# Optimization experiments

Measured on AMD Instinct MI355X. Metric: run time of the kernel, lower is better.

## Reference

```python
import jax, jax.numpy as jnp
import numpy as np

B, T, C, H, L = 1024, 20, 512, 8, 8
V, BS = 2, 32
D = C // H
EPS = 1e-5


def setup_inputs() -> dict:
    key = jax.random.key(0)
    ks = iter(jax.random.split(key, 16))
    n = lambda shape, s=0.02: jax.random.normal(next(ks), shape, dtype=jnp.float32) * s
    return {
        "x": jax.random.normal(next(ks), (B, T, V), dtype=jnp.float32),
        "enc_w": n((V, C)), "enc_b": jnp.zeros((C,), jnp.float32),
        "wpe": n((BS, C)),
        "ln1_w": jnp.ones((L, C), jnp.float32), "ln1_b": jnp.zeros((L, C), jnp.float32),
        "attn_w": n((L, C, 3 * C)), "attn_b": jnp.zeros((L, 3 * C), jnp.float32),
        "proj_w": n((L, C, C), 0.02 / np.sqrt(2 * L)), "proj_b": jnp.zeros((L, C), jnp.float32),
        "ln2_w": jnp.ones((L, C), jnp.float32), "ln2_b": jnp.zeros((L, C), jnp.float32),
        "fc1_w": n((L, C, 4 * C)), "fc1_b": jnp.zeros((L, 4 * C), jnp.float32),
        "fc2_w": n((L, 4 * C, C), 0.02 / np.sqrt(2 * L)), "fc2_b": jnp.zeros((L, C), jnp.float32),
        "lnf_w": jnp.ones((C,), jnp.float32), "lnf_b": jnp.zeros((C,), jnp.float32),
        "pred_w": n((C, V)), "pred_b": jnp.zeros((V,), jnp.float32),
    }


def _ln(x, w, b):
    mu = x.mean(-1, keepdims=True)
    var = x.var(-1, keepdims=True)  # biased, matches torch LayerNorm
    return (x - mu) * jax.lax.rsqrt(var + EPS) * w + b


def _forward(x, enc_w, enc_b, wpe, ln1_w, ln1_b, attn_w, attn_b, proj_w, proj_b,
             ln2_w, ln2_b, fc1_w, fc1_b, fc2_w, fc2_b, lnf_w, lnf_b, pred_w, pred_b):
    # traj_encoder_1 + positional embeddings (pos = arange(1, T+1), T != 9)
    h = x @ enc_w + enc_b + wpe[1:T + 1]
    mask = jnp.tril(jnp.ones((T, T), bool))  # causal mask
    scale = 1.0 / np.sqrt(D)

    def block(h, p):
        l1w, l1b, aw, ab, pw, pb, l2w, l2b, f1w, f1b, f2w, f2b = p
        qkv = _ln(h, l1w, l1b) @ aw + ab          # [B,T,3C]
        q, k, v = jnp.split(qkv, 3, axis=-1)
        q = q.reshape(B, T, H, D).transpose(0, 2, 1, 3)
        k = k.reshape(B, T, H, D).transpose(0, 2, 1, 3)
        v = v.reshape(B, T, H, D).transpose(0, 2, 1, 3)
        att = jnp.einsum('bhqd,bhkd->bhqk', q, k) * scale
        att = jnp.where(mask, att, -jnp.inf)
        att = jax.nn.softmax(att, axis=-1)
        y = jnp.einsum('bhqk,bhkd->bhqd', att, v)
        y = y.transpose(0, 2, 1, 3).reshape(B, T, C)
        h = h + y @ pw + pb
        m = _ln(h, l2w, l2b)
        h = h + jax.nn.gelu(m @ f1w + f1b, approximate=False) @ f2w + f2b
        return h, None

    params = (ln1_w, ln1_b, attn_w, attn_b, proj_w, proj_b,
              ln2_w, ln2_b, fc1_w, fc1_b, fc2_w, fc2_b)
    h, _ = jax.lax.scan(block, h, params)
    feat = _ln(h, lnf_w, lnf_b)
    return feat @ pred_w + pred_b  # predictor_1 -> [B,T,2]


def reference(x, enc_w, enc_b, wpe, ln1_w, ln1_b, attn_w, attn_b, proj_w, proj_b,
              ln2_w, ln2_b, fc1_w, fc1_b, fc2_w, fc2_b, lnf_w, lnf_b, pred_w, pred_b):
    return _forward(x, enc_w, enc_b, wpe, ln1_w, ln1_b, attn_w, attn_b, proj_w, proj_b,
                    ln2_w, ln2_b, fc1_w, fc1_b, fc2_w, fc2_b, lnf_w, lnf_b, pred_w, pred_b)
```

## Files before the change

### kernel.cpp

```cpp
#include <hip/hip_runtime.h>
#include <hip/hip_bf16.h>
#include <math.h>

#define NB 1024
#define NT 20
#define NC 512
#define NH 8
#define NL 8
#define MTOK (NB*NT)

using bf16 = __hip_bfloat16;
typedef float f32x4 __attribute__((ext_vector_type(4)));
typedef short s16x8 __attribute__((ext_vector_type(8)));

static __device__ __forceinline__ float us2f(unsigned short u) {
    union { float f; unsigned int i; } c; c.i = ((unsigned int)u) << 16; return c.f;
}
static __device__ __forceinline__ unsigned short f2bfu(float x) {
    union { bf16 b; unsigned short u; } c; c.b = __float2bfloat16(x); return c.u;
}
static __device__ __forceinline__ bf16 f2bf(float x) { return __float2bfloat16(x); }

static __device__ __forceinline__ void cp16(const bf16* g, bf16* lds_base, int lane) {
#if __has_builtin(__builtin_amdgcn_global_load_lds)
    __builtin_amdgcn_global_load_lds(
        (const __attribute__((address_space(1))) unsigned int*)g,
        (__attribute__((address_space(3))) unsigned int*)lds_base, 16, 0, 0);
#else
    ((int4*)lds_base)[lane] = *(const int4*)g;
#endif
}

static __device__ __forceinline__ void sync_sched() {
#if __has_builtin(__builtin_amdgcn_sched_barrier)
    __builtin_amdgcn_sched_barrier(0);
#endif
}

static __device__ __forceinline__ float gelu_f(float v) {
    return v * __builtin_amdgcn_rcpf(
        1.0f + __expf(-1.5957691f * v * (1.0f + 0.044715f * v * v)));
}

__global__ __launch_bounds__(256) void enc_kernel(
    const float* __restrict__ x, const float* __restrict__ ew,
    const float* __restrict__ eb, const float* __restrict__ wpe,
    float* __restrict__ h) {
    int idx = blockIdx.x * 256 + threadIdx.x;
    int token = idx >> 7, c4 = idx & 127;
    int t = token % NT;
    float x0 = x[(size_t)token * 2], x1 = x[(size_t)token * 2 + 1];
    const float4* w4 = (const float4*)ew;
    float4 w0 = w4[c4], w1 = w4[128 + c4];
    float4 b = ((const float4*)eb)[c4];
    float4 pe = ((const float4*)(wpe + (size_t)(t + 1) * NC))[c4];
    float4 o;
    o.x = x0 * w0.x + x1 * w1.x + b.x + pe.x;
    o.y = x0 * w0.y + x1 * w1.y + b.y + pe.y;
    o.z = x0 * w0.z + x1 * w1.z + b.z + pe.z;
    o.w = x0 * w0.w + x1 * w1.w + b.w + pe.w;
    ((float4*)h)[idx] = o;
}

__global__ __launch_bounds__(256) void wconv_kernel(
    const float* __restrict__ in, bf16* __restrict__ out, int K, int N) {
    __shared__ float tile[32][33];
    int z = blockIdx.z;
    int k0 = blockIdx.x * 32, n0 = blockIdx.y * 32;
    int tx = threadIdx.x & 31, ty = threadIdx.x >> 5;
    const float* src = in + (size_t)z * K * N;
    bf16* dst = out + (size_t)z * K * N;
#pragma unroll
    for (int i = 0; i < 4; ++i)
        tile[ty + i * 8][tx] = src[(size_t)(k0 + ty + i * 8) * N + n0 + tx];
    __syncthreads();
#pragma unroll
    for (int i = 0; i < 4; ++i)
        dst[(size_t)(n0 + ty + i * 8) * K + k0 + tx] = f2bf(tile[tx][ty + i * 8]);
}

__global__ __launch_bounds__(256) void ln_kernel(
    const float* __restrict__ h, const float* __restrict__ w,
    const float* __restrict__ b, bf16* __restrict__ out) {
    int lane = threadIdx.x & 63, wave = threadIdx.x >> 6;
    int token = blockIdx.x * 4 + wave;
    const float4* row = (const float4*)(h + (size_t)token * NC);
    float4 v0 = row[lane], v1 = row[lane + 64];
    float s  = v0.x + v0.y + v0.z + v0.w + v1.x + v1.y + v1.z + v1.w;
    float sq = v0.x*v0.x + v0.y*v0.y + v0.z*v0.z + v0.w*v0.w
             + v1.x*v1.x + v1.y*v1.y + v1.z*v1.z + v1.w*v1.w;
#pragma unroll
    for (int off = 32; off; off >>= 1) {
        s  += __shfl_xor(s, off, 64);
        sq += __shfl_xor(sq, off, 64);
    }
    float mean = s * (1.0f / NC);
    float var = sq * (1.0f / NC) - mean * mean;
    float rstd = rsqrtf(var + 1e-5f);
    const float4* w4 = (const float4*)w;
    const float4* b4 = (const float4*)b;
    float4 wa = w4[lane], wb = w4[lane + 64];
    float4 ba = b4[lane], bb = b4[lane + 64];
    ushort4 o0, o1;
    o0.x = f2bfu((v0.x - mean) * rstd * wa.x + ba.x);
    o0.y = f2bfu((v0.y - mean) * rstd * wa.y + ba.y);
    o0.z = f2bfu((v0.z - mean) * rstd * wa.z + ba.z);
    o0.w = f2bfu((v0.w - mean) * rstd * wa.w + ba.w);
    o1.x = f2bfu((v1.x - mean) * rstd * wb.x + bb.x);
    o1.y = f2bfu((v1.y - mean) * rstd * wb.y + bb.y);
    o1.z = f2bfu((v1.z - mean) * rstd * wb.z + bb.z);
    o1.w = f2bfu((v1.w - mean) * rstd * wb.w + bb.w);
    *(ushort4*)(out + (size_t)token * NC + lane * 4) = o0;
    *(ushort4*)(out + (size_t)token * NC + 256 + lane * 4) = o1;
}

__global__ __launch_bounds__(256) void addln_kernel(
    float* __restrict__ h, const bf16* __restrict__ delta,
    const float* __restrict__ w, const float* __restrict__ b,
    bf16* __restrict__ out) {
    int lane = threadIdx.x & 63, wave = threadIdx.x >> 6;
    int token = blockIdx.x * 4 + wave;
    float4* row = (float4*)(h + (size_t)token * NC);
    float4 v0 = row[lane], v1 = row[lane + 64];
    const ushort4* drow = (const ushort4*)(delta + (size_t)token * NC);
    ushort4 d0 = drow[lane], d1 = drow[lane + 64];
    v0.x += us2f(d0.x); v0.y += us2f(d0.y); v0.z += us2f(d0.z); v0.w += us2f(d0.w);
    v1.x += us2f(d1.x); v1.y += us2f(d1.y); v1.z += us2f(d1.z); v1.w += us2f(d1.w);
    row[lane] = v0; row[lane + 64] = v1;
    float s  = v0.x + v0.y + v0.z + v0.w + v1.x + v1.y + v1.z + v1.w;
    float sq = v0.x*v0.x + v0.y*v0.y + v0.z*v0.z + v0.w*v0.w
             + v1.x*v1.x + v1.y*v1.y + v1.z*v1.z + v1.w*v1.w;
#pragma unroll
    for (int off = 32; off; off >>= 1) {
        s  += __shfl_xor(s, off, 64);
        sq += __shfl_xor(sq, off, 64);
    }
    float mean = s * (1.0f / NC);
    float var = sq * (1.0f / NC) - mean * mean;
    float rstd = rsqrtf(var + 1e-5f);
    const float4* w4 = (const float4*)w;
    const float4* b4 = (const float4*)b;
    float4 wa = w4[lane], wb = w4[lane + 64];
    float4 ba = b4[lane], bb = b4[lane + 64];
    ushort4 o0, o1;
    o0.x = f2bfu((v0.x - mean) * rstd * wa.x + ba.x);
    o0.y = f2bfu((v0.y - mean) * rstd * wa.y + ba.y);
    o0.z = f2bfu((v0.z - mean) * rstd * wa.z + ba.z);
    o0.w = f2bfu((v0.w - mean) * rstd * wa.w + ba.w);
    o1.x = f2bfu((v1.x - mean) * rstd * wb.x + bb.x);
    o1.y = f2bfu((v1.y - mean) * rstd * wb.y + bb.y);
    o1.z = f2bfu((v1.z - mean) * rstd * wb.z + bb.z);
    o1.w = f2bfu((v1.w - mean) * rstd * wb.w + bb.w);
    *(ushort4*)(out + (size_t)token * NC + lane * 4) = o0;
    *(ushort4*)(out + (size_t)token * NC + 256 + lane * 4) = o1;
}

template <int EPI>
__global__ __launch_bounds__(256) void gemm_a(
    const bf16* __restrict__ A, const bf16* __restrict__ Wt,
    const float* __restrict__ bias, bf16* __restrict__ outb, int N, int K) {
    __shared__ __align__(16) bf16 lB[2][128 * 32];
    const int tid = threadIdx.x;
    const int lane = tid & 63;
    const int wave = tid >> 6;

    const int flat = blockIdx.y * gridDim.x + blockIdx.x;
    const int per = (gridDim.x * gridDim.y) >> 3;
    const int nid = (flat & 7) * per + (flat >> 3);
    const int mt = nid / gridDim.x;
    const int nt = nid - mt * gridDim.x;
    const int m0 = mt * 128, n0 = nt * 128;

    f32x4 acc[2][8] = {};

    const int c0 = tid, c1 = tid + 256;
    const int r0 = c0 >> 2, q0 = (((c0 & 3) ^ ((r0 >> 1) & 3)) * 8);
    const int r1 = c1 >> 2, q1 = (((c1 & 3) ^ ((r1 >> 1) & 3)) * 8);
    const bf16* Bb = Wt + (size_t)n0 * K;

    const int fm = lane & 15;
    const int fk8 = (lane >> 4) * 8;
    const int fkS = (((lane >> 4) ^ ((fm >> 1) & 3)) * 8);
    const int iters = K / 32;

    const bf16* Arow0 = A + (size_t)(m0 + wave * 32 + fm) * K + fk8;
    const bf16* Arow1 = Arow0 + (size_t)16 * K;

    auto stageB = [&](int kk, int buf) {
        cp16(Bb + (size_t)r0 * K + kk + q0, &lB[buf][(wave * 64) * 8], lane);
        cp16(Bb + (size_t)r1 * K + kk + q1, &lB[buf][(256 + wave * 64) * 8], lane);
    };
    s16x8 a0 = *(const s16x8*)Arow0;
    s16x8 a1 = *(const s16x8*)Arow1;
    stageB(0, 0);
    for (int it = 0; it < iters; ++it) {
        const int cur = it & 1;
        const int kn = (it + 1 < iters) ? (it + 1) * 32 : 0;
        __builtin_amdgcn_s_barrier();
        s16x8 an0 = *(const s16x8*)(Arow0 + kn);
        s16x8 an1 = *(const s16x8*)(Arow1 + kn);
        stageB(kn, cur ^ 1);
        sync_sched();
        __builtin_amdgcn_s_waitcnt(0xF74);
        __builtin_amdgcn_s_barrier();
        sync_sched();

        s16x8 bfr[8];
#pragma unroll
        for (int ni = 0; ni < 8; ++ni)
            bfr[ni] = *(const s16x8*)&lB[cur][(ni * 16 + fm) * 32 + fkS];
#pragma unroll
        for (int ni = 0; ni < 8; ++ni)
            acc[0][ni] = __builtin_amdgcn_mfma_f32_16x16x32_bf16(a0, bfr[ni], acc[0][ni], 0, 0, 0);
#pragma unroll
        for (int ni = 0; ni < 8; ++ni)
            acc[1][ni] = __builtin_amdgcn_mfma_f32_16x16x32_bf16(a1, bfr[ni], acc[1][ni], 0, 0, 0);
        a0 = an0; a1 = an1;
    }

    const int er = lane >> 4;
    const int ec = lane & 15;
#pragma unroll
    for (int mi = 0; mi < 2; ++mi) {
#pragma unroll
        for (int ni = 0; ni < 8; ++ni) {
            int col = n0 + ni * 16 + ec;
            float bcol = bias[col];
#pragma unroll
            for (int r = 0; r < 4; ++r) {
                int row = m0 + wave * 32 + mi * 16 + er * 4 + r;
                float v = acc[mi][ni][r] + bcol;
                size_t idx = (size_t)row * N + col;
                if (EPI == 0) outb[idx] = f2bf(v);
                else          outb[idx] = f2bf(gelu_f(v));
            }
        }
    }
}

__global__ __launch_bounds__(256) void gemm64_a(
    const bf16* __restrict__ A, const bf16* __restrict__ Wt,
    const float* __restrict__ bias, bf16* __restrict__ outb, int N, int K) {
    __shared__ __align__(16) bf16 lB[2][64 * 32];
    const int tid = threadIdx.x;
    const int lane = tid & 63;
    const int wave = tid >> 6;

    const int flat = blockIdx.y * gridDim.x + blockIdx.x;
    const int per = (gridDim.x * gridDim.y) >> 3;
    const int nid = (flat & 7) * per + (flat >> 3);
    const int mt = nid / gridDim.x;
    const int nt = nid - mt * gridDim.x;
    const int m0 = mt * 128, n0 = nt * 64;

    f32x4 acc[2][4] = {};

    const int c0 = tid;
    const int r0 = c0 >> 2, q0 = (((c0 & 3) ^ ((r0 >> 1) & 3)) * 8);
    const bf16* Bb = Wt + (size_t)n0 * K;

    const int fm = lane & 15;
    const int fk8 = (lane >> 4) * 8;
    const int fkS = (((lane >> 4) ^ ((fm >> 1) & 3)) * 8);
    const int iters = K / 32;

    const bf16* Arow0 = A + (size_t)(m0 + wave * 32 + fm) * K + fk8;
    const bf16* Arow1 = Arow0 + (size_t)16 * K;

    auto stageB = [&](int kk, int buf) {
        cp16(Bb + (size_t)r0 * K + kk + q0, &lB[buf][(wave * 64) * 8], lane);
    };
    s16x8 a0 = *(const s16x8*)Arow0;
    s16x8 a1 = *(const s16x8*)Arow1;
    stageB(0, 0);
    for (int it = 0; it < iters; ++it) {
        const int cur = it & 1;
        const int kn = (it + 1 < iters) ? (it + 1) * 32 : 0;
        __builtin_amdgcn_s_barrier();
        s16x8 an0 = *(const s16x8*)(Arow0 + kn);
        s16x8 an1 = *(const s16x8*)(Arow1 + kn);
        stageB(kn, cur ^ 1);
        sync_sched();
        __builtin_amdgcn_s_waitcnt(0xF73);
        __builtin_amdgcn_s_barrier();
        sync_sched();

        s16x8 bfr[4];
#pragma unroll
        for (int ni = 0; ni < 4; ++ni)
            bfr[ni] = *(const s16x8*)&lB[cur][(ni * 16 + fm) * 32 + fkS];
#pragma unroll
        for (int ni = 0; ni < 4; ++ni)
            acc[0][ni] = __builtin_amdgcn_mfma_f32_16x16x32_bf16(a0, bfr[ni], acc[0][ni], 0, 0, 0);
#pragma unroll
        for (int ni = 0; ni < 4; ++ni)
            acc[1][ni] = __builtin_amdgcn_mfma_f32_16x16x32_bf16(a1, bfr[ni], acc[1][ni], 0, 0, 0);
        a0 = an0; a1 = an1;
    }

    const int er = lane >> 4;
    const int ec = lane & 15;
#pragma unroll
    for (int mi = 0; mi < 2; ++mi) {
#pragma unroll
        for (int ni = 0; ni < 4; ++ni) {
            int col = n0 + ni * 16 + ec;
            float bcol = bias[col];
#pragma unroll
            for (int r = 0; r < 4; ++r) {
                int row = m0 + wave * 32 + mi * 16 + er * 4 + r;
                float v = acc[mi][ni][r] + bcol;
                outb[(size_t)row * N + col] = f2bf(v);
            }
        }
    }
}

__global__ __launch_bounds__(64) void attn_kernel(
    const bf16* __restrict__ qkv, bf16* __restrict__ y) {
    __shared__ __align__(16) float qs[NT][68];
    __shared__ __align__(16) float ks[NT][68];
    __shared__ float vT[64][21];
    __shared__ __align__(16) float P[NT][24];
    const int lane = threadIdx.x;
    const int b = blockIdx.x >> 3, hh = blockIdx.x & 7;
    const bf16* base = qkv + (size_t)b * NT * (3 * NC) + hh * 64;

    for (int idx = lane; idx < NT * 32; idx += 64) {
        int t = idx >> 5, d2 = (idx & 31) * 2;
        const unsigned short* p;
        p = (const unsigned short*)(base + (size_t)t * (3 * NC) + d2);
        qs[t][d2] = us2f(p[0]); qs[t][d2 + 1] = us2f(p[1]);
        p = (const unsigned short*)(base + (size_t)t * (3 * NC) + NC + d2);
        ks[t][d2] = us2f(p[0]); ks[t][d2 + 1] = us2f(p[1]);
        p = (const unsigned short*)(base + (size_t)t * (3 * NC) + 2 * NC + d2);
        vT[d2][t] = us2f(p[0]); vT[d2 + 1][t] = us2f(p[1]);
    }
    __syncthreads();

    for (int pp = lane; pp < NT * NT; pp += 64) {
        int i = (int)(((unsigned)pp * 52429u) >> 20);
        int j = pp - i * 20;
        const float4* qi = (const float4*)qs[i];
        const float4* kj = (const float4*)ks[j];
        float s = 0.0f;
#pragma unroll
        for (int d4 = 0; d4 < 16; ++d4) {
            float4 a = qi[d4], c = kj[d4];
            s += a.x * c.x + a.y * c.y + a.z * c.z + a.w * c.w;
        }
        P[i][j] = s * 0.125f;
    }
    __syncthreads();

    if (lane < NT) {
        int i = lane;
        float m = -INFINITY;
        for (int j = 0; j <= i; ++j) m = fmaxf(m, P[i][j]);
        float sum = 0.0f;
        for (int j = 0; j <= i; ++j) { float e = __expf(P[i][j] - m); P[i][j] = e; sum += e; }
        float inv = 1.0f / sum;
        for (int j = 0; j <= i; ++j) P[i][j] *= inv;
        for (int j = i + 1; j < NT; ++j) P[i][j] = 0.0f;
    }
    __syncthreads();

    float vr[NT];
#pragma unroll
    for (int j = 0; j < NT; ++j) vr[j] = vT[lane][j];
    bf16* yb = y + (size_t)b * NT * NC + hh * 64;
#pragma unroll
    for (int i = 0; i < NT; ++i) {
        const float4* pr = (const float4*)P[i];
        float o = 0.0f;
#pragma unroll
        for (int j4 = 0; j4 < 5; ++j4) {
            float4 pv = pr[j4];
            o += pv.x * vr[j4 * 4] + pv.y * vr[j4 * 4 + 1]
               + pv.z * vr[j4 * 4 + 2] + pv.w * vr[j4 * 4 + 3];
        }
        yb[(size_t)i * NC + lane] = f2bf(o);
    }
}

__global__ __launch_bounds__(256) void lnf_pred_kernel(
    const float* __restrict__ h, const bf16* __restrict__ delta,
    const float* __restrict__ w, const float* __restrict__ b,
    const float* __restrict__ pw, const float* __restrict__ pb,
    float* __restrict__ out) {
    int lane = threadIdx.x & 63, wave = threadIdx.x >> 6;
    int token = blockIdx.x * 4 + wave;
    const float4* row = (const float4*)(h + (size_t)token * NC);
    float4 v0 = row[lane], v1 = row[lane + 64];
    const ushort4* drow = (const ushort4*)(delta + (size_t)token * NC);
    ushort4 d0 = drow[lane], d1 = drow[lane + 64];
    v0.x += us2f(d0.x); v0.y += us2f(d0.y); v0.z += us2f(d0.z); v0.w += us2f(d0.w);
    v1.x += us2f(d1.x); v1.y += us2f(d1.y); v1.z += us2f(d1.z); v1.w += us2f(d1.w);
    float s  = v0.x + v0.y + v0.z + v0.w + v1.x + v1.y + v1.z + v1.w;
    float sq = v0.x*v0.x + v0.y*v0.y + v0.z*v0.z + v0.w*v0.w
             + v1.x*v1.x + v1.y*v1.y + v1.z*v1.z + v1.w*v1.w;
#pragma unroll
    for (int off = 32; off; off >>= 1) {
        s  += __shfl_xor(s, off, 64);
        sq += __shfl_xor(sq, off, 64);
    }
    float mean = s * (1.0f / NC);
    float var = sq * (1.0f / NC) - mean * mean;
    float rstd = rsqrtf(var + 1e-5f);
    const float4* w4 = (const float4*)w;
    const float4* b4 = (const float4*)b;
    float4 wa = w4[lane], wb = w4[lane + 64];
    float4 ba = b4[lane], bb = b4[lane + 64];
    const float2* pw2 = (const float2*)pw;
    float a0 = 0.0f, a1 = 0.0f;
    int c = lane * 4;
    float f; float2 pv;
    f = (v0.x - mean) * rstd * wa.x + ba.x; pv = pw2[c + 0]; a0 += f * pv.x; a1 += f * pv.y;
    f = (v0.y - mean) * rstd * wa.y + ba.y; pv = pw2[c + 1]; a0 += f * pv.x; a1 += f * pv.y;
    f = (v0.z - mean) * rstd * wa.z + ba.z; pv = pw2[c + 2]; a0 += f * pv.x; a1 += f * pv.y;
    f = (v0.w - mean) * rstd * wa.w + ba.w; pv = pw2[c + 3]; a0 += f * pv.x; a1 += f * pv.y;
    c = 256 + lane * 4;
    f = (v1.x - mean) * rstd * wb.x + bb.x; pv = pw2[c + 0]; a0 += f * pv.x; a1 += f * pv.y;
    f = (v1.y - mean) * rstd * wb.y + bb.y; pv = pw2[c + 1]; a0 += f * pv.x; a1 += f * pv.y;
    f = (v1.z - mean) * rstd * wb.z + bb.z; pv = pw2[c + 2]; a0 += f * pv.x; a1 += f * pv.y;
    f = (v1.w - mean) * rstd * wb.w + bb.w; pv = pw2[c + 3]; a0 += f * pv.x; a1 += f * pv.y;
#pragma unroll
    for (int off = 32; off; off >>= 1) {
        a0 += __shfl_xor(a0, off, 64);
        a1 += __shfl_xor(a1, off, 64);
    }
    if (lane == 0) {
        out[(size_t)token * 2]     = a0 + pb[0];
        out[(size_t)token * 2 + 1] = a1 + pb[1];
    }
}

extern "C" void kernel_launch(void* const* d_in, const int* in_sizes, int n_in,
                              void* d_out, int out_size, void* d_ws, size_t ws_size,
                              hipStream_t stream) {
    (void)in_sizes; (void)n_in; (void)out_size; (void)ws_size;
    const float* x      = (const float*)d_in[0];
    const float* enc_w  = (const float*)d_in[1];
    const float* enc_b  = (const float*)d_in[2];
    const float* wpe    = (const float*)d_in[3];
    const float* ln1_w  = (const float*)d_in[4];
    const float* ln1_b  = (const float*)d_in[5];
    const float* attn_w = (const float*)d_in[6];
    const float* attn_b = (const float*)d_in[7];
    const float* proj_w = (const float*)d_in[8];
    const float* proj_b = (const float*)d_in[9];
    const float* ln2_w  = (const float*)d_in[10];
    const float* ln2_b  = (const float*)d_in[11];
    const float* fc1_w  = (const float*)d_in[12];
    const float* fc1_b  = (const float*)d_in[13];
    const float* fc2_w  = (const float*)d_in[14];
    const float* fc2_b  = (const float*)d_in[15];
    const float* lnf_w  = (const float*)d_in[16];
    const float* lnf_b  = (const float*)d_in[17];
    const float* pred_w = (const float*)d_in[18];
    const float* pred_b = (const float*)d_in[19];
    float* out = (float*)d_out;

    char* p = (char*)d_ws;
    float* h  = (float*)p;  p += (size_t)MTOK * NC * 4;
    bf16* xa  = (bf16*)p;   p += (size_t)MTOK * NC * 2;
    bf16* dl  = (bf16*)p;   p += (size_t)MTOK * NC * 2;
    bf16* big = (bf16*)p;   p += (size_t)MTOK * (4 * NC) * 2;
    bf16* aT  = (bf16*)p;   p += (size_t)NL * (3 * NC) * NC * 2;
    bf16* pT  = (bf16*)p;   p += (size_t)NL * NC * NC * 2;
    bf16* f1T = (bf16*)p;   p += (size_t)NL * (4 * NC) * NC * 2;
    bf16* f2T = (bf16*)p;   p += (size_t)NL * NC * (4 * NC) * 2;

    enc_kernel<<<MTOK * 128 / 256, 256, 0, stream>>>(x, enc_w, enc_b, wpe, h);
    wconv_kernel<<<dim3(16, 48, NL), 256, 0, stream>>>(attn_w, aT, NC, 3 * NC);
    wconv_kernel<<<dim3(16, 16, NL), 256, 0, stream>>>(proj_w, pT, NC, NC);
    wconv_kernel<<<dim3(16, 64, NL), 256, 0, stream>>>(fc1_w, f1T, NC, 4 * NC);
    wconv_kernel<<<dim3(64, 16, NL), 256, 0, stream>>>(fc2_w, f2T, 4 * NC, NC);

    for (int l = 0; l < NL; ++l) {
        if (l == 0)
            ln_kernel<<<MTOK / 4, 256, 0, stream>>>(h, ln1_w, ln1_b, xa);
        else
            addln_kernel<<<MTOK / 4, 256, 0, stream>>>(
                h, dl, ln1_w + l * NC, ln1_b + l * NC, xa);
        gemm_a<0><<<dim3(12, 160), 256, 0, stream>>>(
            xa, aT + (size_t)l * 3 * NC * NC, attn_b + l * 3 * NC, big, 3 * NC, NC);
        attn_kernel<<<NB * NH, 64, 0, stream>>>(big, xa);
        gemm64_a<<<dim3(8, 160), 256, 0, stream>>>(
            xa, pT + (size_t)l * NC * NC, proj_b + l * NC, dl, NC, NC);
        addln_kernel<<<MTOK / 4, 256, 0, stream>>>(
            h, dl, ln2_w + l * NC, ln2_b + l * NC, xa);
        gemm_a<2><<<dim3(16, 160), 256, 0, stream>>>(
            xa, f1T + (size_t)l * 4 * NC * NC, fc1_b + l * 4 * NC, big, 4 * NC, NC);
        gemm64_a<<<dim3(8, 160), 256, 0, stream>>>(
            big, f2T + (size_t)l * NC * 4 * NC, fc2_b + l * NC, dl, NC, 4 * NC);
    }
    lnf_pred_kernel<<<MTOK / 4, 256, 0, stream>>>(
        h, dl, lnf_w, lnf_b, pred_w, pred_b, out);
}
```

Measured before the change: 2.838 ms.

## Load GEMM weight fragments directly from global memory into registers, dropping LDS staging

Both GEMM kernels stop staging the weight tile through double-buffered shared memory with global_load_lds and barriers. Each wave now loads its A and B MFMA fragments straight from global memory into registers, using a two-stage register ping-pong unrolled by two. This removes LDS traffic and block-wide barriers, but each of the four waves now reads the same B tile separately. That increases global/L2 load traffic and register pressure.

```diff
diff --git a/kernel.cpp b/kernel.cpp
--- a/kernel.cpp
+++ b/kernel.cpp
@@ -20,22 +20,6 @@
     union { bf16 b; unsigned short u; } c; c.b = __float2bfloat16(x); return c.u;
 }
 static __device__ __forceinline__ bf16 f2bf(float x) { return __float2bfloat16(x); }
-
-static __device__ __forceinline__ void cp16(const bf16* g, bf16* lds_base, int lane) {
-#if __has_builtin(__builtin_amdgcn_global_load_lds)
-    __builtin_amdgcn_global_load_lds(
-        (const __attribute__((address_space(1))) unsigned int*)g,
-        (__attribute__((address_space(3))) unsigned int*)lds_base, 16, 0, 0);
-#else
-    ((int4*)lds_base)[lane] = *(const int4*)g;
-#endif
-}
-
-static __device__ __forceinline__ void sync_sched() {
-#if __has_builtin(__builtin_amdgcn_sched_barrier)
-    __builtin_amdgcn_sched_barrier(0);
-#endif
-}
 
 static __device__ __forceinline__ float gelu_f(float v) {
     return v * __builtin_amdgcn_rcpf(
@@ -156,10 +140,9 @@
 }
 
 template <int EPI>
-__global__ __launch_bounds__(256) void gemm_a(
+__global__ __launch_bounds__(256) void gemm_r(
     const bf16* __restrict__ A, const bf16* __restrict__ Wt,
     const float* __restrict__ bias, bf16* __restrict__ outb, int N, int K) {
-    __shared__ __align__(16) bf16 lB[2][128 * 32];
     const int tid = threadIdx.x;
     const int lane = tid & 63;
     const int wave = tid >> 6;
@@ -171,51 +154,48 @@
     const int nt = nid - mt * gridDim.x;
     const int m0 = mt * 128, n0 = nt * 128;
 
+    const int fm = lane & 15;
+    const int k8 = (lane >> 4) * 8;
+
+    const bf16* Ar0 = A + (size_t)(m0 + wave * 32 + fm) * K + k8;
+    const bf16* Ar1 = Ar0 + (size_t)16 * K;
+    const bf16* Br  = Wt + (size_t)(n0 + fm) * K + k8;
+
     f32x4 acc[2][8] = {};
-
-    const int c0 = tid, c1 = tid + 256;
-    const int r0 = c0 >> 2, q0 = (((c0 & 3) ^ ((r0 >> 1) & 3)) * 8);
-    const int r1 = c1 >> 2, q1 = (((c1 & 3) ^ ((r1 >> 1) & 3)) * 8);
-    const bf16* Bb = Wt + (size_t)n0 * K;
-
-    const int fm = lane & 15;
-    const int fk8 = (lane >> 4) * 8;
-    const int fkS = (((lane >> 4) ^ ((fm >> 1) & 3)) * 8);
+    s16x8 aX[2], bX[8], aY[2], bY[8];
+
+    aX[0] = *(const s16x8*)Ar0;
+    aX[1] = *(const s16x8*)Ar1;
+#pragma unroll
+    for (int ni = 0; ni < 8; ++ni)
+        bX[ni] = *(const s16x8*)(Br + (size_t)ni * 16 * K);
+
     const int iters = K / 32;
-
-    const bf16* Arow0 = A + (size_t)(m0 + wave * 32 + fm) * K + fk8;
-    const bf16* Arow1 = Arow0 + (size_t)16 * K;
-
-    auto stageB = [&](int kk, int buf) {
-        cp16(Bb + (size_t)r0 * K + kk + q0, &lB[buf][(wave * 64) * 8], lane);
-        cp16(Bb + (size_t)r1 * K + kk + q1, &lB[buf][(256 + wave * 64) * 8], lane);
-    };
-    s16x8 a0 = *(const s16x8*)Arow0;
-    s16x8 a1 = *(const s16x8*)Arow1;
-    stageB(0, 0);
-    for (int it = 0; it < iters; ++it) {
-        const int cur = it & 1;
-        const int kn = (it + 1 < iters) ? (it + 1) * 32 : 0;
-        __builtin_amdgcn_s_barrier();
-        s16x8 an0 = *(const s16x8*)(Arow0 + kn);
-        s16x8 an1 = *(const s16x8*)(Arow1 + kn);
-        stageB(kn, cur ^ 1);
-        sync_sched();
-        __builtin_amdgcn_s_waitcnt(0xF74);
-        __builtin_amdgcn_s_barrier();
-        sync_sched();
-
-        s16x8 bfr[8];
-#pragma unroll
-        for (int ni = 0; ni < 8; ++ni)
-            bfr[ni] = *(const s16x8*)&lB[cur][(ni * 16 + fm) * 32 + fkS];
-#pragma unroll
-        for (int ni = 0; ni < 8; ++ni)
-            acc[0][ni] = __builtin_amdgcn_mfma_f32_16x16x32_bf16(a0, bfr[ni], acc[0][ni], 0, 0, 0);
-#pragma unroll
-        for (int ni = 0; ni < 8; ++ni)
-            acc[1][ni] = __builtin_amdgcn_mfma_f32_16x16x32_bf16(a1, bfr[ni], acc[1][ni], 0, 0, 0);
-        a0 = an0; a1 = an1;
+    for (int it = 0; it < iters; it += 2) {
+        const int k1 = (it + 1) * 32;
+        const int k2 = (it + 2 < iters) ? (it + 2) * 32 : 0;
+        aY[0] = *(const s16x8*)(Ar0 + k1);
+        aY[1] = *(const s16x8*)(Ar1 + k1);
+#pragma unroll
+        for (int ni = 0; ni < 8; ++ni)
+            bY[ni] = *(const s16x8*)(Br + (size_t)ni * 16 * K + k1);
+#pragma unroll
+        for (int ni = 0; ni < 8; ++ni)
+            acc[0][ni] = __builtin_amdgcn_mfma_f32_16x16x32_bf16(aX[0], bX[ni], acc[0][ni], 0, 0, 0);
+#pragma unroll
+        for (int ni = 0; ni < 8; ++ni)
+            acc[1][ni] = __builtin_amdgcn_mfma_f32_16x16x32_bf16(aX[1], bX[ni], acc[1][ni], 0, 0, 0);
+        aX[0] = *(const s16x8*)(Ar0 + k2);
+        aX[1] = *(const s16x8*)(Ar1 + k2);
+#pragma unroll
+        for (int ni = 0; ni < 8; ++ni)
+            bX[ni] = *(const s16x8*)(Br + (size_t)ni * 16 * K + k2);
+#pragma unroll
+        for (int ni = 0; ni < 8; ++ni)
+            acc[0][ni] = __builtin_amdgcn_mfma_f32_16x16x32_bf16(aY[0], bY[ni], acc[0][ni], 0, 0, 0);
+#pragma unroll
+        for (int ni = 0; ni < 8; ++ni)
+            acc[1][ni] = __builtin_amdgcn_mfma_f32_16x16x32_bf16(aY[1], bY[ni], acc[1][ni], 0, 0, 0);
     }
 
     const int er = lane >> 4;
@@ -238,10 +218,9 @@
     }
 }
 
-__global__ __launch_bounds__(256) void gemm64_a(
+__global__ __launch_bounds__(256) void gemm64_r(
     const bf16* __restrict__ A, const bf16* __restrict__ Wt,
     const float* __restrict__ bias, bf16* __restrict__ outb, int N, int K) {
-    __shared__ __align__(16) bf16 lB[2][64 * 32];
     const int tid = threadIdx.x;
     const int lane = tid & 63;
     const int wave = tid >> 6;
@@ -253,49 +232,48 @@
     const int nt = nid - mt * gridDim.x;
     const int m0 = mt * 128, n0 = nt * 64;
 
+    const int fm = lane & 15;
+    const int k8 = (lane >> 4) * 8;
+
+    const bf16* Ar0 = A + (size_t)(m0 + wave * 32 + fm) * K + k8;
+    const bf16* Ar1 = Ar0 + (size_t)16 * K;
+    const bf16* Br  = Wt + (size_t)(n0 + fm) * K + k8;
+
     f32x4 acc[2][4] = {};
-
-    const int c0 = tid;
-    const int r0 = c0 >> 2, q0 = (((c0 & 3) ^ ((r0 >> 1) & 3)) * 8);
-    const bf16* Bb = Wt + (size_t)n0 * K;
-
-    const int fm = lane & 15;
-    const int fk8 = (lane >> 4) * 8;
-    const int fkS = (((lane >> 4) ^ ((fm >> 1) & 3)) * 8);
+    s16x8 aX[2], bX[4], aY[2], bY[4];
+
+    aX[0] = *(const s16x8*)Ar0;
+    aX[1] = *(const s16x8*)Ar1;
+#pragma unroll
+    for (int ni = 0; ni < 4; ++ni)
+        bX[ni] = *(const s16x8*)(Br + (size_t)ni * 16 * K);
+
     const int iters = K / 32;
-
-    const bf16* Arow0 = A + (size_t)(m0 + wave * 32 + fm) * K + fk8;
-    const bf16* Arow1 = Arow0 + (size_t)16 * K;
-
-    auto stageB = [&](int kk, int buf) {
-        cp16(Bb + (size_t)r0 * K + kk + q0, &lB[buf][(wave * 64) * 8], lane);
-    };
-    s16x8 a0 = *(const s16x8*)Arow0;
-    s16x8 a1 = *(const s16x8*)Arow1;
-    stageB(0, 0);
-    for (int it = 0; it < iters; ++it) {
-        const int cur = it & 1;
-        const int kn = (it + 1 < iters) ? (it + 1) * 32 : 0;
-        __builtin_amdgcn_s_barrier();
-        s16x8 an0 = *(const s16x8*)(Arow0 + kn);
-        s16x8 an1 = *(const s16x8*)(Arow1 + kn);
-        stageB(kn, cur ^ 1);
-        sync_sched();
-        __builtin_amdgcn_s_waitcnt(0xF73);
-        __builtin_amdgcn_s_barrier();
-        sync_sched();
-
-        s16x8 bfr[4];
-#pragma unroll
-        for (int ni = 0; ni < 4; ++ni)
-            bfr[ni] = *(const s16x8*)&lB[cur][(ni * 16 + fm) * 32 + fkS];
-#pragma unroll
-        for (int ni = 0; ni < 4; ++ni)
-            acc[0][ni] = __builtin_amdgcn_mfma_f32_16x16x32_bf16(a0, bfr[ni], acc[0][ni], 0, 0, 0);
-#pragma unroll
-        for (int ni = 0; ni < 4; ++ni)
-            acc[1][ni] = __builtin_amdgcn_mfma_f32_16x16x32_bf16(a1, bfr[ni], acc[1][ni], 0, 0, 0);
-        a0 = an0; a1 = an1;
+    for (int it = 0; it < iters; it += 2) {
+        const int k1 = (it + 1) * 32;
+        const int k2 = (it + 2 < iters) ? (it + 2) * 32 : 0;
+        aY[0] = *(const s16x8*)(Ar0 + k1);
+        aY[1] = *(const s16x8*)(Ar1 + k1);
+#pragma unroll
+        for (int ni = 0; ni < 4; ++ni)
+            bY[ni] = *(const s16x8*)(Br + (size_t)ni * 16 * K + k1);
+#pragma unroll
+        for (int ni = 0; ni < 4; ++ni)
+            acc[0][ni] = __builtin_amdgcn_mfma_f32_16x16x32_bf16(aX[0], bX[ni], acc[0][ni], 0, 0, 0);
+#pragma unroll
+        for (int ni = 0; ni < 4; ++ni)
+            acc[1][ni] = __builtin_amdgcn_mfma_f32_16x16x32_bf16(aX[1], bX[ni], acc[1][ni], 0, 0, 0);
+        aX[0] = *(const s16x8*)(Ar0 + k2);
+        aX[1] = *(const s16x8*)(Ar1 + k2);
+#pragma unroll
+        for (int ni = 0; ni < 4; ++ni)
+            bX[ni] = *(const s16x8*)(Br + (size_t)ni * 16 * K + k2);
+#pragma unroll
+        for (int ni = 0; ni < 4; ++ni)
+            acc[0][ni] = __builtin_amdgcn_mfma_f32_16x16x32_bf16(aY[0], bY[ni], acc[0][ni], 0, 0, 0);
+#pragma unroll
+        for (int ni = 0; ni < 4; ++ni)
+            acc[1][ni] = __builtin_amdgcn_mfma_f32_16x16x32_bf16(aY[1], bY[ni], acc[1][ni], 0, 0, 0);
     }
 
     const int er = lane >> 4;
@@ -483,16 +461,16 @@
         else
             addln_kernel<<<MTOK / 4, 256, 0, stream>>>(
                 h, dl, ln1_w + l * NC, ln1_b + l * NC, xa);
-        gemm_a<0><<<dim3(12, 160), 256, 0, stream>>>(
+        gemm_r<0><<<dim3(12, 160), 256, 0, stream>>>(
             xa, aT + (size_t)l * 3 * NC * NC, attn_b + l * 3 * NC, big, 3 * NC, NC);
         attn_kernel<<<NB * NH, 64, 0, stream>>>(big, xa);
-        gemm64_a<<<dim3(8, 160), 256, 0, stream>>>(
+        gemm64_r<<<dim3(8, 160), 256, 0, stream>>>(
             xa, pT + (size_t)l * NC * NC, proj_b + l * NC, dl, NC, NC);
         addln_kernel<<<MTOK / 4, 256, 0, stream>>>(
             h, dl, ln2_w + l * NC, ln2_b + l * NC, xa);
-        gemm_a<2><<<dim3(16, 160), 256, 0, stream>>>(
+        gemm_r<2><<<dim3(16, 160), 256, 0, stream>>>(
             xa, f1T + (size_t)l * 4 * NC * NC, fc1_b + l * 4 * NC, big, 4 * NC, NC);
-        gemm64_a<<<dim3(8, 160), 256, 0, stream>>>(
+        gemm64_r<<<dim3(8, 160), 256, 0, stream>>>(
             big, f2T + (size_t)l * NC * 4 * NC, fc2_b + l * NC, dl, NC, 4 * NC);
     }
     lnf_pred_kernel<<<MTOK / 4, 256, 0, stream>>>(
```

Result: slower. 5.946 ms (+109.5%).

## Stage A operand through LDS and use 2x2 wave tiling in GEMMs

Applied to the files above, without the earlier changes.

Both GEMM kernels now stage the activation (A) tile into double-buffered LDS with async global-to-LDS copies, instead of each wave loading its A fragments straight from global memory into registers. The 128x128 GEMM switches from four waves each owning 32 full-width rows to a 2x2 wave grid with 64x64 per wave. The aim is coalesced A loads shared through LDS and a better MFMA-to-LDS-read ratio. In exchange, LDS usage per block roughly doubles, which can reduce occupancy, and the register-level prefetch of A is dropped.

```diff
diff --git a/kernel.cpp b/kernel.cpp
--- a/kernel.cpp
+++ b/kernel.cpp
@@ -156,13 +156,15 @@
 }
 
 template <int EPI>
-__global__ __launch_bounds__(256) void gemm_a(
+__global__ __launch_bounds__(256) void gemm(
     const bf16* __restrict__ A, const bf16* __restrict__ Wt,
     const float* __restrict__ bias, bf16* __restrict__ outb, int N, int K) {
+    __shared__ __align__(16) bf16 lA[2][128 * 32];
     __shared__ __align__(16) bf16 lB[2][128 * 32];
     const int tid = threadIdx.x;
     const int lane = tid & 63;
     const int wave = tid >> 6;
+    const int wm = wave >> 1, wn = wave & 1;
 
     const int flat = blockIdx.y * gridDim.x + blockIdx.x;
     const int per = (gridDim.x * gridDim.y) >> 3;
@@ -171,64 +173,60 @@
     const int nt = nid - mt * gridDim.x;
     const int m0 = mt * 128, n0 = nt * 128;
 
-    f32x4 acc[2][8] = {};
+    f32x4 acc[4][4] = {};
 
     const int c0 = tid, c1 = tid + 256;
     const int r0 = c0 >> 2, q0 = (((c0 & 3) ^ ((r0 >> 1) & 3)) * 8);
     const int r1 = c1 >> 2, q1 = (((c1 & 3) ^ ((r1 >> 1) & 3)) * 8);
+    const bf16* Ab = A + (size_t)m0 * K;
     const bf16* Bb = Wt + (size_t)n0 * K;
 
     const int fm = lane & 15;
-    const int fk8 = (lane >> 4) * 8;
-    const int fkS = (((lane >> 4) ^ ((fm >> 1) & 3)) * 8);
+    const int fk = (((lane >> 4) ^ ((fm >> 1) & 3)) * 8);
     const int iters = K / 32;
 
-    const bf16* Arow0 = A + (size_t)(m0 + wave * 32 + fm) * K + fk8;
-    const bf16* Arow1 = Arow0 + (size_t)16 * K;
-
-    auto stageB = [&](int kk, int buf) {
+    auto stage = [&](int kk, int buf) {
+        cp16(Ab + (size_t)r0 * K + kk + q0, &lA[buf][(wave * 64) * 8], lane);
+        cp16(Ab + (size_t)r1 * K + kk + q1, &lA[buf][(256 + wave * 64) * 8], lane);
         cp16(Bb + (size_t)r0 * K + kk + q0, &lB[buf][(wave * 64) * 8], lane);
         cp16(Bb + (size_t)r1 * K + kk + q1, &lB[buf][(256 + wave * 64) * 8], lane);
     };
-    s16x8 a0 = *(const s16x8*)Arow0;
-    s16x8 a1 = *(const s16x8*)Arow1;
-    stageB(0, 0);
+    stage(0, 0);
     for (int it = 0; it < iters; ++it) {
         const int cur = it & 1;
         const int kn = (it + 1 < iters) ? (it + 1) * 32 : 0;
         __builtin_amdgcn_s_barrier();
-        s16x8 an0 = *(const s16x8*)(Arow0 + kn);
-        s16x8 an1 = *(const s16x8*)(Arow1 + kn);
-        stageB(kn, cur ^ 1);
-        sync_sched();
+        stage(kn, cur ^ 1);
         __builtin_amdgcn_s_waitcnt(0xF74);
         __builtin_amdgcn_s_barrier();
         sync_sched();
 
-        s16x8 bfr[8];
-#pragma unroll
-        for (int ni = 0; ni < 8; ++ni)
-            bfr[ni] = *(const s16x8*)&lB[cur][(ni * 16 + fm) * 32 + fkS];
-#pragma unroll
-        for (int ni = 0; ni < 8; ++ni)
-            acc[0][ni] = __builtin_amdgcn_mfma_f32_16x16x32_bf16(a0, bfr[ni], acc[0][ni], 0, 0, 0);
-#pragma unroll
-        for (int ni = 0; ni < 8; ++ni)
-            acc[1][ni] = __builtin_amdgcn_mfma_f32_16x16x32_bf16(a1, bfr[ni], acc[1][ni], 0, 0, 0);
-        a0 = an0; a1 = an1;
+        s16x8 af[4], bfr[4];
+#pragma unroll
+        for (int mi = 0; mi < 4; ++mi)
+            af[mi] = *(const s16x8*)&lA[cur][(wm * 64 + mi * 16 + fm) * 32 + fk];
+#pragma unroll
+        for (int ni = 0; ni < 4; ++ni)
+            bfr[ni] = *(const s16x8*)&lB[cur][(wn * 64 + ni * 16 + fm) * 32 + fk];
+#pragma unroll
+        for (int mi = 0; mi < 4; ++mi)
+#pragma unroll
+            for (int ni = 0; ni < 4; ++ni)
+                acc[mi][ni] = __builtin_amdgcn_mfma_f32_16x16x32_bf16(
+                    af[mi], bfr[ni], acc[mi][ni], 0, 0, 0);
     }
 
     const int er = lane >> 4;
     const int ec = lane & 15;
 #pragma unroll
-    for (int mi = 0; mi < 2; ++mi) {
-#pragma unroll
-        for (int ni = 0; ni < 8; ++ni) {
-            int col = n0 + ni * 16 + ec;
+    for (int mi = 0; mi < 4; ++mi) {
+#pragma unroll
+        for (int ni = 0; ni < 4; ++ni) {
+            int col = n0 + wn * 64 + ni * 16 + ec;
             float bcol = bias[col];
 #pragma unroll
             for (int r = 0; r < 4; ++r) {
-                int row = m0 + wave * 32 + mi * 16 + er * 4 + r;
+                int row = m0 + wm * 64 + mi * 16 + er * 4 + r;
                 float v = acc[mi][ni][r] + bcol;
                 size_t idx = (size_t)row * N + col;
                 if (EPI == 0) outb[idx] = f2bf(v);
@@ -238,9 +236,10 @@
     }
 }
 
-__global__ __launch_bounds__(256) void gemm64_a(
+__global__ __launch_bounds__(256) void gemm64(
     const bf16* __restrict__ A, const bf16* __restrict__ Wt,
     const float* __restrict__ bias, bf16* __restrict__ outb, int N, int K) {
+    __shared__ __align__(16) bf16 lA[2][128 * 32];
     __shared__ __align__(16) bf16 lB[2][64 * 32];
     const int tid = threadIdx.x;
     const int lane = tid & 63;
@@ -255,47 +254,44 @@
 
     f32x4 acc[2][4] = {};
 
-    const int c0 = tid;
+    const int c0 = tid, c1 = tid + 256;
     const int r0 = c0 >> 2, q0 = (((c0 & 3) ^ ((r0 >> 1) & 3)) * 8);
+    const int r1 = c1 >> 2, q1 = (((c1 & 3) ^ ((r1 >> 1) & 3)) * 8);
+    const bf16* Ab = A + (size_t)m0 * K;
     const bf16* Bb = Wt + (size_t)n0 * K;
 
     const int fm = lane & 15;
-    const int fk8 = (lane >> 4) * 8;
-    const int fkS = (((lane >> 4) ^ ((fm >> 1) & 3)) * 8);
+    const int fk = (((lane >> 4) ^ ((fm >> 1) & 3)) * 8);
     const int iters = K / 32;
 
-    const bf16* Arow0 = A + (size_t)(m0 + wave * 32 + fm) * K + fk8;
-    const bf16* Arow1 = Arow0 + (size_t)16 * K;
-
-    auto stageB = [&](int kk, int buf) {
+    auto stage = [&](int kk, int buf) {
+        cp16(Ab + (size_t)r0 * K + kk + q0, &lA[buf][(wave * 64) * 8], lane);
+        cp16(Ab + (size_t)r1 * K + kk + q1, &lA[buf][(256 + wave * 64) * 8], lane);
         cp16(Bb + (size_t)r0 * K + kk + q0, &lB[buf][(wave * 64) * 8], lane);
     };
-    s16x8 a0 = *(const s16x8*)Arow0;
-    s16x8 a1 = *(const s16x8*)Arow1;
-    stageB(0, 0);
+    stage(0, 0);
     for (int it = 0; it < iters; ++it) {
         const int cur = it & 1;
         const int kn = (it + 1 < iters) ? (it + 1) * 32 : 0;
         __builtin_amdgcn_s_barrier();
-        s16x8 an0 = *(const s16x8*)(Arow0 + kn);
-        s16x8 an1 = *(const s16x8*)(Arow1 + kn);
-        stageB(kn, cur ^ 1);
-        sync_sched();
+        stage(kn, cur ^ 1);
         __builtin_amdgcn_s_waitcnt(0xF73);
         __builtin_amdgcn_s_barrier();
         sync_sched();
 
-        s16x8 bfr[4];
+        s16x8 af[2], bfr[4];
+#pragma unroll
+        for (int mi = 0; mi < 2; ++mi)
+            af[mi] = *(const s16x8*)&lA[cur][(wave * 32 + mi * 16 + fm) * 32 + fk];
 #pragma unroll
         for (int ni = 0; ni < 4; ++ni)
-            bfr[ni] = *(const s16x8*)&lB[cur][(ni * 16 + fm) * 32 + fkS];
-#pragma unroll
-        for (int ni = 0; ni < 4; ++ni)
-            acc[0][ni] = __builtin_amdgcn_mfma_f32_16x16x32_bf16(a0, bfr[ni], acc[0][ni], 0, 0, 0);
-#pragma unroll
-        for (int ni = 0; ni < 4; ++ni)
-            acc[1][ni] = __builtin_amdgcn_mfma_f32_16x16x32_bf16(a1, bfr[ni], acc[1][ni], 0, 0, 0);
-        a0 = an0; a1 = an1;
+            bfr[ni] = *(const s16x8*)&lB[cur][(ni * 16 + fm) * 32 + fk];
+#pragma unroll
+        for (int mi = 0; mi < 2; ++mi)
+#pragma unroll
+            for (int ni = 0; ni < 4; ++ni)
+                acc[mi][ni] = __builtin_amdgcn_mfma_f32_16x16x32_bf16(
+                    af[mi], bfr[ni], acc[mi][ni], 0, 0, 0);
     }
 
     const int er = lane >> 4;
@@ -483,16 +479,16 @@
         else
             addln_kernel<<<MTOK / 4, 256, 0, stream>>>(
                 h, dl, ln1_w + l * NC, ln1_b + l * NC, xa);
-        gemm_a<0><<<dim3(12, 160), 256, 0, stream>>>(
+        gemm<0><<<dim3(12, 160), 256, 0, stream>>>(
             xa, aT + (size_t)l * 3 * NC * NC, attn_b + l * 3 * NC, big, 3 * NC, NC);
         attn_kernel<<<NB * NH, 64, 0, stream>>>(big, xa);
-        gemm64_a<<<dim3(8, 160), 256, 0, stream>>>(
+        gemm64<<<dim3(8, 160), 256, 0, stream>>>(
             xa, pT + (size_t)l * NC * NC, proj_b + l * NC, dl, NC, NC);
         addln_kernel<<<MTOK / 4, 256, 0, stream>>>(
             h, dl, ln2_w + l * NC, ln2_b + l * NC, xa);
-        gemm_a<2><<<dim3(16, 160), 256, 0, stream>>>(
+        gemm<2><<<dim3(16, 160), 256, 0, stream>>>(
             xa, f1T + (size_t)l * 4 * NC * NC, fc1_b + l * 4 * NC, big, 4 * NC, NC);
-        gemm64_a<<<dim3(8, 160), 256, 0, stream>>>(
+        gemm64<<<dim3(8, 160), 256, 0, stream>>>(
             big, f2T + (size_t)l * NC * 4 * NC, fc2_b + l * NC, dl, NC, 4 * NC);
     }
     lnf_pred_kernel<<<MTOK / 4, 256, 0, stream>>>(
```

Result: faster. 2.544 ms (-10.3%).
